# Optimization experiments

Hardware: AMD Instinct MI355X
Metric: run time of the kernel (lower is better)

## Reference

```python
import jax, jax.numpy as jnp
import numpy as np
from jax import lax

N = 64          # padded / uniform graph size
B = 512         # number of graph pairs
E = 512         # edges per graph
GCN_SIZES = [64, 32, 16]
CONV_OUT = [8, 16, 32]
D_IN = 16


def gcn_conv(x, src, dst, W, b):
    # PyG GCNConv: add self-loops, symmetric norm D^-1/2 (A+I) D^-1/2, then XW + b
    n = x.shape[0]
    h = x @ W
    deg = jnp.zeros((n,), x.dtype).at[dst].add(1.0) + 1.0  # +1 self-loop
    dinv = lax.rsqrt(deg)
    msg = h[src] * (dinv[src] * dinv[dst])[:, None]
    agg = jnp.zeros_like(h).at[dst].add(msg) + h * (dinv * dinv)[:, None]
    return agg + b


def gcn_pass(x, ei, Ws, bs):
    src, dst = ei[0], ei[1]
    feats = []
    h = x
    for i in range(len(Ws)):
        h = gcn_conv(h, src, dst, Ws[i], bs[i])
        feats.append(h)               # pre-ReLU features are used for similarity
        if i < len(Ws) - 1:
            h = jax.nn.relu(h)        # dropout p used in eval -> identity
    return feats


def conv_same(x, w, b):
    y = lax.conv_general_dilated(x, w, (1, 1), 'SAME',
                                 dimension_numbers=('NCHW', 'OIHW', 'NCHW'))
    return y + b[None, :, None, None]


def maxpool2(x):
    return lax.reduce_window(x, -jnp.inf, lax.max, (1, 1, 2, 2), (1, 1, 2, 2), 'VALID')


def setup_inputs() -> dict:
    key = jax.random.key(0)
    ks = jax.random.split(key, 32)
    f32 = jnp.float32
    x_q = jax.random.normal(ks[0], (B * N, D_IN), f32)
    x_c = jax.random.normal(ks[1], (B * N, D_IN), f32)
    off = (jnp.arange(B, dtype=jnp.int32) * N)[:, None]
    eq_s = (jax.random.randint(ks[2], (B, E), 0, N, jnp.int32) + off).reshape(-1)
    eq_d = (jax.random.randint(ks[3], (B, E), 0, N, jnp.int32) + off).reshape(-1)
    ec_s = (jax.random.randint(ks[4], (B, E), 0, N, jnp.int32) + off).reshape(-1)
    ec_d = (jax.random.randint(ks[5], (B, E), 0, N, jnp.int32) + off).reshape(-1)
    edge_q = jnp.stack([eq_s, eq_d])
    edge_c = jnp.stack([ec_s, ec_d])

    def lin(k, fi, fo):
        return jax.random.normal(k, (fi, fo), f32) / np.sqrt(fi)

    inp = dict(x_q=x_q, x_c=x_c, edge_q=edge_q, edge_c=edge_c)
    dims = [D_IN] + GCN_SIZES
    for i in range(3):
        inp[f'gcn_w{i+1}'] = lin(ks[6 + i], dims[i], dims[i + 1])
        inp[f'gcn_b{i+1}'] = jnp.zeros((dims[i + 1],), f32)
    cin = [1] + CONV_OUT[:-1]
    for i in range(3):
        fan = cin[i] * 25
        inp[f'conv_w{i+1}'] = jax.random.normal(ks[10 + i], (3, CONV_OUT[i], cin[i], 5, 5), f32) / np.sqrt(fan)
        inp[f'conv_b{i+1}'] = jnp.zeros((3, CONV_OUT[i]), f32)
    inp['lin_w1'] = lin(ks[14], 6144, 256)
    inp['lin_b1'] = jnp.zeros((256,), f32)
    inp['lin_w2'] = lin(ks[15], 256, 16)
    inp['lin_b2'] = jnp.zeros((16,), f32)
    inp['score_w'] = lin(ks[16], 16, 1)
    inp['score_b'] = jnp.zeros((1,), f32)
    return inp


def _forward(x_q, x_c, gcn_w1, gcn_b1, gcn_w2, gcn_b2, gcn_w3, gcn_b3,
             conv_w1, conv_b1, conv_w2, conv_b2, conv_w3, conv_b3,
             lin_w1, lin_b1, lin_w2, lin_b2, score_w, score_b,
             edge_q, edge_c):
    Ws = (gcn_w1, gcn_w2, gcn_w3)
    bs = (gcn_b1, gcn_b2, gcn_b3)
    qf = gcn_pass(x_q, edge_q, Ws, bs)   # list of [B*N, d_i]
    cf = gcn_pass(x_c, edge_c, Ws, bs)
    sims = [jnp.einsum('bnd,bmd->bnm', q.reshape(B, N, -1), c.reshape(B, N, -1))
            for q, c in zip(qf, cf)]
    cw = (conv_w1, conv_w2, conv_w3)
    cb = (conv_b1, conv_b2, conv_b3)
    outs = []
    for m in range(3):                    # separate conv weights per similarity matrix
        z = sims[m][:, None]              # [B, 1, N, N]
        for l in range(3):
            z = maxpool2(jax.nn.relu(conv_same(z, cw[l][m], cb[l][m])))
        outs.append(z)                    # [B, 32, 8, 8]
    feat = jnp.concatenate(outs, axis=1).reshape(B, 6144)
    h = jax.nn.relu(feat @ lin_w1 + lin_b1)
    h = jax.nn.relu(h @ lin_w2 + lin_b2)
    return (h @ score_w + score_b).reshape(-1)  # is_sig=False -> logits [B]


def reference(x_q, x_c, edge_q, edge_c, gcn_w1, gcn_b1, gcn_w2, gcn_b2, gcn_w3, gcn_b3,
              conv_w1, conv_b1, conv_w2, conv_b2, conv_w3, conv_b3,
              lin_w1, lin_b1, lin_w2, lin_b2, score_w, score_b):
    return _forward(x_q, x_c, gcn_w1, gcn_b1, gcn_w2, gcn_b2, gcn_w3, gcn_b3,
                    conv_w1, conv_b1, conv_w2, conv_b2, conv_w3, conv_b3,
                    lin_w1, lin_b1, lin_w2, lin_b2, score_w, score_b,
                    edge_q, edge_c)
```

## Files before the change

### kernel.cpp

```cpp
#include <hip/hip_runtime.h>
#include <hip/hip_bf16.h>

constexpr int B = 512, N = 64, E = 512, NE = B * E;

typedef __attribute__((ext_vector_type(8))) short bf8v;
typedef __attribute__((ext_vector_type(4))) float f32x4;
typedef unsigned short u16;

__device__ __forceinline__ u16 f2bf(float f) {
  unsigned u = __builtin_bit_cast(unsigned, f);
  u += 0x7FFFu + ((u >> 16) & 1u);
  return (u16)(u >> 16);
}

__device__ __forceinline__ int cmin(int a, int b) { return a < b ? a : b; }

template <int DIN, int DOUT, int NR, int NC, bool STORE_NEXT>
__device__ __forceinline__ void gcn_layer(
    float* __restrict__ At, float* __restrict__ Xt, float* __restrict__ Hs,
    const float* __restrict__ W, const float* __restrict__ bias,
    u16* __restrict__ fout, int g, int t) {
  constexpr int XS = 68;
  constexpr int CT = DOUT / NC;
  static_assert((64 / NR) * CT == 512, "thread mapping");
  const int ct = t % CT, nt = t / CT;
  const int n0 = NR * nt, c0 = NC * ct;
  {
    float acc[NR][NC] = {};
#pragma unroll 4
    for (int k = 0; k < DIN; ++k) {
      float xa[NR];
      if constexpr (NR == 4) {
        float4 xv = *(const float4*)&Xt[k * XS + n0];
        xa[0] = xv.x; xa[1] = xv.y; xa[2] = xv.z; xa[3] = xv.w;
      } else {
        float2 xv = *(const float2*)&Xt[k * XS + n0];
        xa[0] = xv.x; xa[1] = xv.y;
      }
      float wa[NC];
      if constexpr (NC == 2) {
        float2 wv = *(const float2*)&W[k * DOUT + c0];
        wa[0] = wv.x; wa[1] = wv.y;
      } else {
        wa[0] = W[k * DOUT + c0];
      }
#pragma unroll
      for (int i = 0; i < NR; ++i)
#pragma unroll
        for (int j = 0; j < NC; ++j) acc[i][j] += xa[i] * wa[j];
    }
#pragma unroll
    for (int i = 0; i < NR; ++i) {
      if constexpr (NC == 2)
        *(float2*)&Hs[(n0 + i) * XS + c0] = make_float2(acc[i][0], acc[i][1]);
      else
        Hs[(n0 + i) * XS + c0] = acc[i][0];
    }
  }
  __syncthreads();
  {
    float acc[NR][NC] = {};
#pragma unroll 4
    for (int s = 0; s < N; ++s) {
      float aa[NR];
      if constexpr (NR == 4) {
        float4 av = *(const float4*)&At[s * XS + n0];
        aa[0] = av.x; aa[1] = av.y; aa[2] = av.z; aa[3] = av.w;
      } else {
        float2 av = *(const float2*)&At[s * XS + n0];
        aa[0] = av.x; aa[1] = av.y;
      }
      float ha[NC];
      if constexpr (NC == 2) {
        float2 hv = *(const float2*)&Hs[s * XS + c0];
        ha[0] = hv.x; ha[1] = hv.y;
      } else {
        ha[0] = Hs[s * XS + c0];
      }
#pragma unroll
      for (int i = 0; i < NR; ++i)
#pragma unroll
        for (int j = 0; j < NC; ++j) acc[i][j] += aa[i] * ha[j];
    }
    float bv[NC];
#pragma unroll
    for (int j = 0; j < NC; ++j) bv[j] = bias[c0 + j];
#pragma unroll
    for (int i = 0; i < NR; ++i) {
      float st[NC];
#pragma unroll
      for (int j = 0; j < NC; ++j) st[j] = acc[i][j] + bv[j];
      if constexpr (NC == 2) {
        unsigned pack = (unsigned)f2bf(st[0]) | ((unsigned)f2bf(st[1]) << 16);
        *(unsigned*)&fout[(size_t)g * N * DOUT + (size_t)(n0 + i) * DOUT + c0] = pack;
      } else {
        fout[(size_t)g * N * DOUT + (size_t)(n0 + i) * DOUT + c0] = f2bf(st[0]);
      }
      if (STORE_NEXT) {
#pragma unroll
        for (int j = 0; j < NC; ++j)
          Xt[(c0 + j) * XS + n0 + i] = fmaxf(st[j], 0.f);
      }
    }
  }
  __syncthreads();
}

__global__ __launch_bounds__(512) void gcn_fused(
    const float* __restrict__ xq, const float* __restrict__ xc,
    const float* __restrict__ W1, const float* __restrict__ b1,
    const float* __restrict__ W2, const float* __restrict__ b2,
    const float* __restrict__ W3, const float* __restrict__ b3,
    const int* __restrict__ eq, const int* __restrict__ ec,
    u16* __restrict__ f1q, u16* __restrict__ f1c,
    u16* __restrict__ f2q, u16* __restrict__ f2c,
    u16* __restrict__ f3q, u16* __restrict__ f3c) {
  constexpr int XS = 68;
  __shared__ __align__(16) float At[N * XS];
  __shared__ __align__(16) float Xt[N * XS];
  __shared__ __align__(16) float Hs[N * XS];
  __shared__ float dl[N];
  __shared__ int cnt[N];
  const int g = blockIdx.x, t = threadIdx.x;
  const float* x = blockIdx.y ? xc : xq;
  const int* edges = blockIdx.y ? ec : eq;
  u16* o1 = blockIdx.y ? f1c : f1q;
  u16* o2 = blockIdx.y ? f2c : f2q;
  u16* o3 = blockIdx.y ? f3c : f3q;
  for (int i = t; i < N * 16; i += 512) {
    int n = i / 16, k = i % 16;
    Xt[k * XS + n] = x[(size_t)g * N * 16 + i];
  }
  for (int i = t; i < N * XS; i += 512) At[i] = 0.f;
  if (t < N) cnt[t] = 1;
  __syncthreads();
  const int* srcp = edges + (size_t)g * E;
  const int* dstp = edges + NE + (size_t)g * E;
  for (int j = t; j < E; j += 512) atomicAdd(&cnt[dstp[j] & 63], 1);
  __syncthreads();
  if (t < N) dl[t] = rsqrtf((float)cnt[t]);
  __syncthreads();
  for (int j = t; j < E; j += 512) {
    int s = srcp[j] & 63, d = dstp[j] & 63;
    atomicAdd(&At[s * XS + d], dl[s] * dl[d]);
  }
  if (t < N) atomicAdd(&At[t * XS + t], dl[t] * dl[t]);
  __syncthreads();
  gcn_layer<16, 64, 4, 2, true>(At, Xt, Hs, W1, b1, o1, g, t);
  gcn_layer<64, 32, 4, 1, true>(At, Xt, Hs, W2, b2, o2, g, t);
  gcn_layer<32, 16, 2, 1, false>(At, Xt, Hs, W3, b3, o3, g, t);
}

__global__ __launch_bounds__(256, 4) void simconv1(
    const u16* __restrict__ f1q, const u16* __restrict__ f1c,
    const u16* __restrict__ f2q, const u16* __restrict__ f2c,
    const u16* __restrict__ f3q, const u16* __restrict__ f3c,
    const float* __restrict__ w, const float* __restrict__ bias,
    u16* __restrict__ out) {
  constexpr int PS = 68, QS = 72;
  __shared__ __align__(16) u16 Qs[64 * QS];
  __shared__ __align__(16) u16 Cs[64 * QS];
  __shared__ __align__(16) float simp[68 * 68];
  __shared__ float wls[25 * 8];
  __shared__ float bls[8];
  const int b = blockIdx.x, m = blockIdx.y, t = threadIdx.x;
  for (int i = t; i < 68 * 68; i += 256) simp[i] = 0.f;
  if (t < 200) {
    int oc = t / 25, tap = t % 25;
    wls[tap * 8 + oc] = w[m * 200 + t];
  }
  if (t < 8) bls[t] = bias[m * 8 + t];
  const u16* fq = (m == 0) ? f1q : (m == 1) ? f2q : f3q;
  const u16* fc = (m == 0) ? f1c : (m == 1) ? f2c : f3c;
  const int D = 64 >> m;
  const int SEG = D >> 3;
  for (int i = t; i < 64 * SEG; i += 256) {
    int n = i / SEG, s = i - n * SEG;
    *(uint4*)&Qs[n * QS + s * 8] = *(const uint4*)&fq[(size_t)b * 64 * D + n * D + s * 8];
    *(uint4*)&Cs[n * QS + s * 8] = *(const uint4*)&fc[(size_t)b * 64 * D + n * D + s * 8];
  }
  if (m == 2 && t < 128) {
    int n = t >> 1, s = t & 1;
    uint4 z = {0u, 0u, 0u, 0u};
    *(uint4*)&Qs[n * QS + 16 + s * 8] = z;
    *(uint4*)&Cs[n * QS + 16 + s * 8] = z;
  }
  __syncthreads();
  const int w4 = t >> 6, lane = t & 63;
  const int r16 = lane & 15, kg = lane >> 4;
  const int Kpad = (m == 0) ? 64 : 32;
#pragma unroll 1
  for (int ct = 0; ct < 4; ++ct) {
    f32x4 acc = {0.f, 0.f, 0.f, 0.f};
    for (int ks = 0; ks < Kpad; ks += 32) {
      bf8v a = *(const bf8v*)&Qs[(w4 * 16 + r16) * QS + ks + kg * 8];
      bf8v bb = *(const bf8v*)&Cs[(ct * 16 + r16) * QS + ks + kg * 8];
      acc = __builtin_amdgcn_mfma_f32_16x16x32_bf16(a, bb, acc, 0, 0, 0);
    }
#pragma unroll
    for (int j = 0; j < 4; ++j)
      simp[(w4 * 16 + kg * 4 + j + 2) * PS + ct * 16 + r16 + 2] = acc[j];
  }
  __syncthreads();
  const int gy = t >> 4, gx = t & 15;
  float pr[8][8];
#pragma unroll
  for (int yy = 0; yy < 8; ++yy) {
    float4 a = *(const float4*)&simp[(4 * gy + yy) * PS + 4 * gx];
    float4 bb = *(const float4*)&simp[(4 * gy + yy) * PS + 4 * gx + 4];
    pr[yy][0] = a.x; pr[yy][1] = a.y; pr[yy][2] = a.z; pr[yy][3] = a.w;
    pr[yy][4] = bb.x; pr[yy][5] = bb.y; pr[yy][6] = bb.z; pr[yy][7] = bb.w;
  }
  u16* op = out + (size_t)(b * 3 + m) * 8192;
#pragma unroll 1
  for (int p2 = 0; p2 < 4; ++p2) {
    float acc[2][16];
#pragma unroll
    for (int p = 0; p < 16; ++p) { acc[0][p] = 0.f; acc[1][p] = 0.f; }
#pragma unroll
    for (int ky = 0; ky < 5; ++ky)
#pragma unroll
      for (int kx = 0; kx < 5; ++kx) {
        float2 wv = *(const float2*)&wls[(ky * 5 + kx) * 8 + p2 * 2];
#pragma unroll
        for (int dy = 0; dy < 4; ++dy)
#pragma unroll
          for (int dx = 0; dx < 4; ++dx) {
            float rv = pr[ky + dy][kx + dx];
            acc[0][dy * 4 + dx] += rv * wv.x;
            acc[1][dy * 4 + dx] += rv * wv.y;
          }
      }
    float b0 = bls[p2 * 2], b1 = bls[p2 * 2 + 1];
#pragma unroll
    for (int ay = 0; ay < 2; ++ay)
#pragma unroll
      for (int ax = 0; ax < 2; ++ax) {
        float v0 = fmaxf(fmaxf(acc[0][(2 * ay) * 4 + 2 * ax], acc[0][(2 * ay) * 4 + 2 * ax + 1]),
                         fmaxf(acc[0][(2 * ay + 1) * 4 + 2 * ax], acc[0][(2 * ay + 1) * 4 + 2 * ax + 1]));
        float v1 = fmaxf(fmaxf(acc[1][(2 * ay) * 4 + 2 * ax], acc[1][(2 * ay) * 4 + 2 * ax + 1]),
                         fmaxf(acc[1][(2 * ay + 1) * 4 + 2 * ax], acc[1][(2 * ay + 1) * 4 + 2 * ax + 1]));
        v0 = fmaxf(v0 + b0, 0.f);
        v1 = fmaxf(v1 + b1, 0.f);
        unsigned pack = (unsigned)f2bf(v0) | ((unsigned)f2bf(v1) << 16);
        *(unsigned*)&op[(size_t)(((2 * gy + ay) * 32) + (2 * gx + ax)) * 8 + p2 * 2] = pack;
      }
  }
}

__global__ __launch_bounds__(256) void prep_kernel(
    const float* __restrict__ lw1, const float* __restrict__ cw2,
    const float* __restrict__ cw3, u16* __restrict__ wT,
    u16* __restrict__ w2p, u16* __restrict__ w3p) {
  const int t = threadIdx.x;
  if (blockIdx.x < 384) {
    __shared__ float tile[64][65];
    const int k0 = (blockIdx.x % 96) * 64, c0 = (blockIdx.x / 96) * 64;
    for (int i = t; i < 4096; i += 256) {
      int r = i >> 6, c = i & 63;
      tile[r][c] = lw1[(size_t)(k0 + r) * 256 + c0 + c];
    }
    __syncthreads();
    for (int i = t; i < 4096; i += 256) {
      int c = i >> 6, k = i & 63;
      wT[(size_t)(c0 + c) * 6144 + k0 + k] = f2bf(tile[k][c]);
    }
    return;
  }
  int i = (blockIdx.x - 384) * 256 + t;
  if (i < 3 * 7 * 16 * 40) {
    int m = i / 4480, r = i % 4480;
    int k = r % 40, rest = r / 40, oc = rest & 15, st = rest >> 4;
    u16 v = 0;
    if (k < 32) {
      int sl = k >> 3, ci = k & 7, tap = st * 4 + sl;
      if (tap < 25) v = f2bf(cw2[((size_t)(m * 16 + oc) * 8 + ci) * 25 + tap]);
    }
    w2p[i] = v;
  }
  if (i < 3 * 26 * 16 * 40) {
    int m = i / 16640, r = i % 16640;
    int k = r % 40, rest = r / 40, oc16 = rest & 15, sthalf = rest >> 4;
    int half = sthalf & 1, st = sthalf >> 1;
    u16 v = 0;
    if (k < 32) {
      int sl = k >> 4, ci = k & 15, tap = st * 2 + sl;
      int oc = half * 16 + oc16;
      if (tap < 25) v = f2bf(cw3[((size_t)(m * 32 + oc) * 16 + ci) * 25 + tap]);
    }
    w3p[i] = v;
  }
}

__global__ __launch_bounds__(256) void conv23_mfma(
    const u16* __restrict__ in, const u16* __restrict__ w2p,
    const float* __restrict__ cb2, const u16* __restrict__ w3p,
    const float* __restrict__ cb3, u16* __restrict__ feat) {
  constexpr int PW2 = 36, PW3 = 20, BS = 40;
  __shared__ __align__(16) u16 uni[16640];
  __shared__ __align__(16) u16 p2s[PW3 * PW3 * 16];
  __shared__ float bls2[16];
  __shared__ float bls3[32];
  const int b = blockIdx.x, m = blockIdx.y, t = threadIdx.x;
  u16* ins2 = uni;
  u16* w2ls = uni + 10368;
  const size_t ibase = (size_t)(b * 3 + m) * 8192;
  for (int i = t; i < PW2 * PW2; i += 256) {
    int y = i / PW2, x = i % PW2;
    uint4 v = {0u, 0u, 0u, 0u};
    if (y >= 2 && y < 34 && x >= 2 && x < 34)
      v = *(const uint4*)&in[ibase + (size_t)((y - 2) * 32 + (x - 2)) * 8];
    *(uint4*)&ins2[i * 8] = v;
  }
  {
    const u16* wsrc = w2p + m * 4480;
    for (int i = t; i < 560; i += 256) *(uint4*)&w2ls[i * 8] = *(const uint4*)&wsrc[i * 8];
  }
  {
    uint4 z = {0u, 0u, 0u, 0u};
    for (int i = t; i < 800; i += 256) *(uint4*)&p2s[i * 8] = z;
  }
  if (t < 16) bls2[t] = cb2[m * 16 + t];
  if (t >= 32 && t < 64) bls3[t - 32] = cb3[m * 32 + (t - 32)];
  __syncthreads();
  const int wv = t >> 6, lane = t & 63;
  const int oc = lane & 15, g = lane >> 4;
  {
    const int xt = wv & 1, ypb = wv >> 1;
    const int x = xt * 16 + oc;
    __builtin_amdgcn_s_setprio(1);
#pragma unroll 1
    for (int grp = 0; grp < 2; ++grp) {
      f32x4 acc[4][2];
#pragma unroll
      for (int i = 0; i < 4; ++i) {
        acc[i][0] = (f32x4){0.f, 0.f, 0.f, 0.f};
        acc[i][1] = (f32x4){0.f, 0.f, 0.f, 0.f};
      }
#pragma unroll
      for (int st = 0; st < 7; ++st) {
        bf8v bvv = *(const bf8v*)&w2ls[(st * 16 + oc) * BS + g * 8];
        const int c0 = cmin(st * 4 + 0, 24), c1 = cmin(st * 4 + 1, 24);
        const int c2 = cmin(st * 4 + 2, 24), c3 = cmin(st * 4 + 3, 24);
        const int k0 = (c0 / 5) * PW2 + c0 % 5, k1 = (c1 / 5) * PW2 + c1 % 5;
        const int k2 = (c2 / 5) * PW2 + c2 % 5, k3 = (c3 / 5) * PW2 + c3 % 5;
        const int koff = (g == 0) ? k0 : (g == 1) ? k1 : (g == 2) ? k2 : k3;
#pragma unroll
        for (int i = 0; i < 4; ++i) {
          const int y0 = 2 * ypb + 4 * (grp * 4 + i);
          const int abase = (y0 * PW2 + x + koff) * 8;
          bf8v a0 = *(const bf8v*)&ins2[abase];
          acc[i][0] = __builtin_amdgcn_mfma_f32_16x16x32_bf16(a0, bvv, acc[i][0], 0, 0, 0);
          bf8v a1 = *(const bf8v*)&ins2[abase + PW2 * 8];
          acc[i][1] = __builtin_amdgcn_mfma_f32_16x16x32_bf16(a1, bvv, acc[i][1], 0, 0, 0);
        }
      }
      const float bb = bls2[oc];
#pragma unroll
      for (int i = 0; i < 4; ++i) {
        const int yp = ypb + 2 * (grp * 4 + i);
        const float v0 = fmaxf(fmaxf(fmaxf(acc[i][0][0], acc[i][0][1]),
                                     fmaxf(acc[i][1][0], acc[i][1][1])) + bb, 0.f);
        const float v1 = fmaxf(fmaxf(fmaxf(acc[i][0][2], acc[i][0][3]),
                                     fmaxf(acc[i][1][2], acc[i][1][3])) + bb, 0.f);
        const int px = xt * 8 + 2 * g;
        p2s[((yp + 2) * PW3 + (px + 2)) * 16 + oc] = f2bf(v0);
        p2s[((yp + 2) * PW3 + (px + 3)) * 16 + oc] = f2bf(v1);
      }
    }
    __builtin_amdgcn_s_setprio(0);
  }
  __syncthreads();
  {
    const u16* wsrc = w3p + m * 16640;
    for (int i = t; i < 2080; i += 256) *(uint4*)&uni[i * 8] = *(const uint4*)&wsrc[i * 8];
  }
  __syncthreads();
  {
    const int sl = g >> 1, ch = (g & 1) * 8;
    const int half = wv & 1, ypb = wv >> 1;
    u16* fb = feat + (size_t)b * 6144 + m * 2048;
    f32x4 acc[4][2];
#pragma unroll
    for (int i = 0; i < 4; ++i) {
      acc[i][0] = (f32x4){0.f, 0.f, 0.f, 0.f};
      acc[i][1] = (f32x4){0.f, 0.f, 0.f, 0.f};
    }
    __builtin_amdgcn_s_setprio(1);
#pragma unroll
    for (int st = 0; st < 13; ++st) {
      bf8v bvv = *(const bf8v*)&uni[(size_t)((st * 2 + half) * 16 + oc) * BS + g * 8];
      const int c0 = cmin(st * 2 + 0, 24), c1 = cmin(st * 2 + 1, 24);
      const int k0 = (c0 / 5) * PW3 + c0 % 5, k1 = (c1 / 5) * PW3 + c1 % 5;
      const int koff = sl ? k1 : k0;
#pragma unroll
      for (int i = 0; i < 4; ++i) {
        const int y0 = 2 * ypb + 4 * i;
        const int abase = (y0 * PW3 + oc + koff) * 16 + ch;
        bf8v a0 = *(const bf8v*)&p2s[abase];
        acc[i][0] = __builtin_amdgcn_mfma_f32_16x16x32_bf16(a0, bvv, acc[i][0], 0, 0, 0);
        bf8v a1 = *(const bf8v*)&p2s[abase + PW3 * 16];
        acc[i][1] = __builtin_amdgcn_mfma_f32_16x16x32_bf16(a1, bvv, acc[i][1], 0, 0, 0);
      }
    }
    __builtin_amdgcn_s_setprio(0);
    const int ocg = half * 16 + oc;
    const float bb = bls3[ocg];
#pragma unroll
    for (int i = 0; i < 4; ++i) {
      const int yp = ypb + 2 * i;
      const float v0 = fmaxf(fmaxf(fmaxf(acc[i][0][0], acc[i][0][1]),
                                   fmaxf(acc[i][1][0], acc[i][1][1])) + bb, 0.f);
      const float v1 = fmaxf(fmaxf(fmaxf(acc[i][0][2], acc[i][0][3]),
                                   fmaxf(acc[i][1][2], acc[i][1][3])) + bb, 0.f);
      unsigned pack = (unsigned)f2bf(v0) | ((unsigned)f2bf(v1) << 16);
      *(unsigned*)&fb[ocg * 64 + yp * 8 + 2 * g] = pack;
    }
  }
}

__global__ __launch_bounds__(256) void lin1_mfma(const u16* __restrict__ feat,
                                                 const u16* __restrict__ wT,
                                                 float* __restrict__ h1p) {
  constexpr int AS = 72;
  __shared__ __align__(16) u16 As[64 * AS];
  __shared__ __align__(16) u16 Bs[64 * AS];
  const int r0 = blockIdx.x * 64, c0 = blockIdx.y * 64, kb = blockIdx.z * 384;
  const int t = threadIdx.x;
  const int w = t >> 6, lane = t & 63;
  const int row16 = lane & 15, kg = lane >> 4;
  f32x4 acc[4] = {{0.f, 0.f, 0.f, 0.f}, {0.f, 0.f, 0.f, 0.f},
                  {0.f, 0.f, 0.f, 0.f}, {0.f, 0.f, 0.f, 0.f}};
  const int lr = t >> 2, lk = (t & 3) * 16;
#pragma unroll 1
  for (int st = 0; st < 6; ++st) {
    __syncthreads();
    const int ks = kb + st * 64;
    {
      const u16* srcA = feat + (size_t)(r0 + lr) * 6144 + ks + lk;
      uint4 a0 = *(const uint4*)srcA;
      uint4 a1 = *(const uint4*)(srcA + 8);
      *(uint4*)&As[lr * AS + lk] = a0;
      *(uint4*)&As[lr * AS + lk + 8] = a1;
      const u16* srcB = wT + (size_t)(c0 + lr) * 6144 + ks + lk;
      uint4 b0 = *(const uint4*)srcB;
      uint4 b1 = *(const uint4*)(srcB + 8);
      *(uint4*)&Bs[lr * AS + lk] = b0;
      *(uint4*)&Bs[lr * AS + lk + 8] = b1;
    }
    __syncthreads();
#pragma unroll
    for (int kk = 0; kk < 2; ++kk) {
      bf8v a = *(const bf8v*)&As[(w * 16 + row16) * AS + kk * 32 + kg * 8];
#pragma unroll
      for (int ct = 0; ct < 4; ++ct) {
        bf8v bb = *(const bf8v*)&Bs[(ct * 16 + row16) * AS + kk * 32 + kg * 8];
        acc[ct] = __builtin_amdgcn_mfma_f32_16x16x32_bf16(a, bb, acc[ct], 0, 0, 0);
      }
    }
  }
  float* out = h1p + (size_t)blockIdx.z * 131072;
#pragma unroll
  for (int ct = 0; ct < 4; ++ct)
#pragma unroll
    for (int j = 0; j < 4; ++j)
      out[(size_t)(r0 + w * 16 + kg * 4 + j) * 256 + c0 + ct * 16 + row16] = acc[ct][j];
}

__global__ __launch_bounds__(256) void head_kernel(
    const float* __restrict__ h1p, const float* __restrict__ b1,
    const float* __restrict__ w2, const float* __restrict__ b2,
    const float* __restrict__ sw, const float* __restrict__ sb,
    float* __restrict__ out) {
  constexpr int HS = 260;
  __shared__ __align__(16) float h1s[16 * HS];
  __shared__ __align__(16) float w2s[256 * 16];
  const int r0 = blockIdx.x * 16, t = threadIdx.x;
  for (int i = t; i < 4096; i += 256) {
    int r = i >> 8, k = i & 255;
    float s = b1[k];
#pragma unroll
    for (int p = 0; p < 16; ++p) s += h1p[(size_t)p * 131072 + (size_t)(r0 + r) * 256 + k];
    h1s[r * HS + k] = s;
    w2s[i] = w2[i];
  }
  __syncthreads();
  const int j = t & 15, r = t >> 4;
  float acc = b2[j];
#pragma unroll 4
  for (int k4 = 0; k4 < 64; ++k4) {
    float4 hv = *(const float4*)&h1s[r * HS + 4 * k4];
    float h0 = fmaxf(hv.x, 0.f), h1v = fmaxf(hv.y, 0.f);
    float h2v = fmaxf(hv.z, 0.f), h3 = fmaxf(hv.w, 0.f);
    acc += h0 * w2s[(4 * k4 + 0) * 16 + j];
    acc += h1v * w2s[(4 * k4 + 1) * 16 + j];
    acc += h2v * w2s[(4 * k4 + 2) * 16 + j];
    acc += h3 * w2s[(4 * k4 + 3) * 16 + j];
  }
  float v = fmaxf(acc, 0.f) * sw[j];
#pragma unroll
  for (int off = 8; off; off >>= 1) v += __shfl_xor(v, off, 16);
  if (j == 0) out[r0 + r] = v + sb[0];
}

extern "C" void kernel_launch(void* const* d_in, const int* in_sizes, int n_in,
                              void* d_out, int out_size, void* d_ws, size_t ws_size,
                              hipStream_t stream) {
  const float* x_q = (const float*)d_in[0];
  const float* x_c = (const float*)d_in[1];
  const int* edge_q = (const int*)d_in[2];
  const int* edge_c = (const int*)d_in[3];
  const float* gw1 = (const float*)d_in[4];
  const float* gb1 = (const float*)d_in[5];
  const float* gw2 = (const float*)d_in[6];
  const float* gb2 = (const float*)d_in[7];
  const float* gw3 = (const float*)d_in[8];
  const float* gb3 = (const float*)d_in[9];
  const float* cw1 = (const float*)d_in[10];
  const float* cb1 = (const float*)d_in[11];
  const float* cw2 = (const float*)d_in[12];
  const float* cb2 = (const float*)d_in[13];
  const float* cw3 = (const float*)d_in[14];
  const float* cb3 = (const float*)d_in[15];
  const float* lw1 = (const float*)d_in[16];
  const float* lb1 = (const float*)d_in[17];
  const float* lw2 = (const float*)d_in[18];
  const float* lb2 = (const float*)d_in[19];
  const float* swt = (const float*)d_in[20];
  const float* sbs = (const float*)d_in[21];
  float* ws = (float*)d_ws;

  const size_t o_f1q = 65536;
  const size_t o_f2q = o_f1q + 2097152;
  const size_t o_f3q = o_f2q + 1048576;
  const size_t o_f1c = o_f3q + 524288;
  const size_t o_f2c = o_f1c + 2097152;
  const size_t o_f3c = o_f2c + 1048576;
  const size_t o_sims = o_f3c + 524288;
  const size_t o_pm1 = o_sims + 6291456;
  const size_t o_pm2 = o_pm1 + 6291456;
  const size_t o_wT = o_pm2 + 3145728;
  const size_t o_w2p = o_wT + 786432;
  const size_t o_w3p = o_w2p + 8192;
  const size_t o_feat = o_sims;
  const size_t o_h1p = o_f1q;

  u16* f1q = (u16*)(ws + o_f1q); u16* f2q = (u16*)(ws + o_f2q); u16* f3q = (u16*)(ws + o_f3q);
  u16* f1c = (u16*)(ws + o_f1c); u16* f2c = (u16*)(ws + o_f2c); u16* f3c = (u16*)(ws + o_f3c);
  u16* pm1 = (u16*)(ws + o_pm1);
  u16* wT = (u16*)(ws + o_wT);
  u16* w2p = (u16*)(ws + o_w2p);
  u16* w3p = (u16*)(ws + o_w3p);
  u16* feat = (u16*)(ws + o_feat);
  float* h1p = ws + o_h1p;

  prep_kernel<<<580, 256, 0, stream>>>(lw1, cw2, cw3, wT, w2p, w3p);

  gcn_fused<<<dim3(B, 2), 512, 0, stream>>>(x_q, x_c, gw1, gb1, gw2, gb2, gw3, gb3,
                                            edge_q, edge_c, f1q, f1c, f2q, f2c, f3q, f3c);

  simconv1<<<dim3(B, 3), 256, 0, stream>>>(f1q, f1c, f2q, f2c, f3q, f3c, cw1, cb1, pm1);

  conv23_mfma<<<dim3(B, 3), 256, 0, stream>>>(pm1, w2p, cb2, w3p, cb3, feat);

  lin1_mfma<<<dim3(8, 4, 16), 256, 0, stream>>>(feat, wT, h1p);
  head_kernel<<<32, 256, 0, stream>>>(h1p, lb1, lw2, lb2, swt, sbs, (float*)d_out);
}
```

Measured before the change: 131.0 us.

## Rewrite fused GCN layers with bf16 MFMA in a 256-thread block

Replaces the scalar fp32 FMA loops for both the XW and the normalized-adjacency matmuls in the GCN kernel with 16x16x32 bf16 MFMA instructions. Adjacency, features and intermediate H are stored in shared memory as bf16 with padded rows, weights are converted and transposed into shared memory per layer, and the block shrinks from 512 to 256 threads. The aim is to cut the ALU cost of the per-graph GCN stage. In exchange, intermediate activations and the adjacency are rounded to bf16, which loses precision, and the per-layer weight staging adds an extra barrier.

```diff
diff --git a/kernel.cpp b/kernel.cpp
--- a/kernel.cpp
+++ b/kernel.cpp
@@ -15,98 +15,59 @@
 
 __device__ __forceinline__ int cmin(int a, int b) { return a < b ? a : b; }
 
-template <int DIN, int DOUT, int NR, int NC, bool STORE_NEXT>
-__device__ __forceinline__ void gcn_layer(
-    float* __restrict__ At, float* __restrict__ Xt, float* __restrict__ Hs,
-    const float* __restrict__ W, const float* __restrict__ bias,
-    u16* __restrict__ fout, int g, int t) {
-  constexpr int XS = 68;
-  constexpr int CT = DOUT / NC;
-  static_assert((64 / NR) * CT == 512, "thread mapping");
-  const int ct = t % CT, nt = t / CT;
-  const int n0 = NR * nt, c0 = NC * ct;
-  {
-    float acc[NR][NC] = {};
-#pragma unroll 4
-    for (int k = 0; k < DIN; ++k) {
-      float xa[NR];
-      if constexpr (NR == 4) {
-        float4 xv = *(const float4*)&Xt[k * XS + n0];
-        xa[0] = xv.x; xa[1] = xv.y; xa[2] = xv.z; xa[3] = xv.w;
-      } else {
-        float2 xv = *(const float2*)&Xt[k * XS + n0];
-        xa[0] = xv.x; xa[1] = xv.y;
-      }
-      float wa[NC];
-      if constexpr (NC == 2) {
-        float2 wv = *(const float2*)&W[k * DOUT + c0];
-        wa[0] = wv.x; wa[1] = wv.y;
-      } else {
-        wa[0] = W[k * DOUT + c0];
-      }
-#pragma unroll
-      for (int i = 0; i < NR; ++i)
-#pragma unroll
-        for (int j = 0; j < NC; ++j) acc[i][j] += xa[i] * wa[j];
-    }
-#pragma unroll
-    for (int i = 0; i < NR; ++i) {
-      if constexpr (NC == 2)
-        *(float2*)&Hs[(n0 + i) * XS + c0] = make_float2(acc[i][0], acc[i][1]);
-      else
-        Hs[(n0 + i) * XS + c0] = acc[i][0];
-    }
-  }
-  __syncthreads();
-  {
-    float acc[NR][NC] = {};
-#pragma unroll 4
-    for (int s = 0; s < N; ++s) {
-      float aa[NR];
-      if constexpr (NR == 4) {
-        float4 av = *(const float4*)&At[s * XS + n0];
-        aa[0] = av.x; aa[1] = av.y; aa[2] = av.z; aa[3] = av.w;
-      } else {
-        float2 av = *(const float2*)&At[s * XS + n0];
-        aa[0] = av.x; aa[1] = av.y;
-      }
-      float ha[NC];
-      if constexpr (NC == 2) {
-        float2 hv = *(const float2*)&Hs[s * XS + c0];
-        ha[0] = hv.x; ha[1] = hv.y;
-      } else {
-        ha[0] = Hs[s * XS + c0];
-      }
-#pragma unroll
-      for (int i = 0; i < NR; ++i)
-#pragma unroll
-        for (int j = 0; j < NC; ++j) acc[i][j] += aa[i] * ha[j];
-    }
-    float bv[NC];
-#pragma unroll
-    for (int j = 0; j < NC; ++j) bv[j] = bias[c0 + j];
-#pragma unroll
-    for (int i = 0; i < NR; ++i) {
-      float st[NC];
-#pragma unroll
-      for (int j = 0; j < NC; ++j) st[j] = acc[i][j] + bv[j];
-      if constexpr (NC == 2) {
-        unsigned pack = (unsigned)f2bf(st[0]) | ((unsigned)f2bf(st[1]) << 16);
-        *(unsigned*)&fout[(size_t)g * N * DOUT + (size_t)(n0 + i) * DOUT + c0] = pack;
-      } else {
-        fout[(size_t)g * N * DOUT + (size_t)(n0 + i) * DOUT + c0] = f2bf(st[0]);
-      }
-      if (STORE_NEXT) {
-#pragma unroll
-        for (int j = 0; j < NC; ++j)
-          Xt[(c0 + j) * XS + n0 + i] = fmaxf(st[j], 0.f);
-      }
-    }
-  }
-  __syncthreads();
-}
-
-__global__ __launch_bounds__(512) void gcn_fused(
+template <int DIN, int KP, int DOUT, bool STORE_NEXT>
+__device__ __forceinline__ void gcn_layer_mfma(
+    const u16* __restrict__ Ab, u16* __restrict__ Xb, u16* __restrict__ Hb,
+    u16* __restrict__ Wb, const float* __restrict__ W,
+    const float* __restrict__ bias, u16* __restrict__ fout, int g, int t) {
+  for (int i = t; i < DOUT * KP; i += 256) {
+    int c = i / KP, k = i % KP;
+    u16 v = 0;
+    if (k < DIN) v = f2bf(W[k * DOUT + c]);
+    Wb[c * 72 + k] = v;
+  }
+  __syncthreads();
+  const int w4 = t >> 6, lane = t & 63;
+  const int r16 = lane & 15, kg = lane >> 4;
+  constexpr int CT = DOUT / 16;
+#pragma unroll
+  for (int ct = 0; ct < CT; ++ct) {
+    f32x4 acc = {0.f, 0.f, 0.f, 0.f};
+#pragma unroll
+    for (int ks = 0; ks < KP; ks += 32) {
+      bf8v a = *(const bf8v*)&Xb[(w4 * 16 + r16) * 72 + ks + kg * 8];
+      bf8v bb = *(const bf8v*)&Wb[(ct * 16 + r16) * 72 + ks + kg * 8];
+      acc = __builtin_amdgcn_mfma_f32_16x16x32_bf16(a, bb, acc, 0, 0, 0);
+    }
+    ushort4 pk;
+    pk.x = f2bf(acc[0]); pk.y = f2bf(acc[1]);
+    pk.z = f2bf(acc[2]); pk.w = f2bf(acc[3]);
+    *(ushort4*)&Hb[(ct * 16 + r16) * 72 + w4 * 16 + kg * 4] = pk;
+  }
+  __syncthreads();
+#pragma unroll
+  for (int ct = 0; ct < CT; ++ct) {
+    f32x4 acc = {0.f, 0.f, 0.f, 0.f};
+#pragma unroll
+    for (int ks = 0; ks < 64; ks += 32) {
+      bf8v a = *(const bf8v*)&Ab[(w4 * 16 + r16) * 72 + ks + kg * 8];
+      bf8v bb = *(const bf8v*)&Hb[(ct * 16 + r16) * 72 + ks + kg * 8];
+      acc = __builtin_amdgcn_mfma_f32_16x16x32_bf16(a, bb, acc, 0, 0, 0);
+    }
+    const int c = ct * 16 + r16;
+    const float bv = bias[c];
+#pragma unroll
+    for (int j = 0; j < 4; ++j) {
+      float st = acc[j] + bv;
+      const int d = w4 * 16 + kg * 4 + j;
+      fout[(size_t)g * N * DOUT + (size_t)d * DOUT + c] = f2bf(st);
+      if (STORE_NEXT) Xb[d * 72 + c] = f2bf(fmaxf(st, 0.f));
+    }
+  }
+  __syncthreads();
+}
+
+__global__ __launch_bounds__(256) void gcn_fused(
     const float* __restrict__ xq, const float* __restrict__ xc,
     const float* __restrict__ W1, const float* __restrict__ b1,
     const float* __restrict__ W2, const float* __restrict__ b2,
@@ -115,40 +76,48 @@
     u16* __restrict__ f1q, u16* __restrict__ f1c,
     u16* __restrict__ f2q, u16* __restrict__ f2c,
     u16* __restrict__ f3q, u16* __restrict__ f3c) {
-  constexpr int XS = 68;
-  __shared__ __align__(16) float At[N * XS];
-  __shared__ __align__(16) float Xt[N * XS];
-  __shared__ __align__(16) float Hs[N * XS];
+  __shared__ __align__(16) float Af[64 * 68];
+  __shared__ __align__(16) u16 Ab[64 * 72];
+  __shared__ __align__(16) u16 Xb[64 * 72];
+  __shared__ __align__(16) u16 Hb[64 * 72];
   __shared__ float dl[N];
   __shared__ int cnt[N];
+  u16* Wb = (u16*)Af;
   const int g = blockIdx.x, t = threadIdx.x;
   const float* x = blockIdx.y ? xc : xq;
   const int* edges = blockIdx.y ? ec : eq;
   u16* o1 = blockIdx.y ? f1c : f1q;
   u16* o2 = blockIdx.y ? f2c : f2q;
   u16* o3 = blockIdx.y ? f3c : f3q;
-  for (int i = t; i < N * 16; i += 512) {
-    int n = i / 16, k = i % 16;
-    Xt[k * XS + n] = x[(size_t)g * N * 16 + i];
-  }
-  for (int i = t; i < N * XS; i += 512) At[i] = 0.f;
+  for (int i = t; i < 64 * 32; i += 256) {
+    int n = i >> 5, k = i & 31;
+    u16 v = 0;
+    if (k < 16) v = f2bf(x[(size_t)g * 1024 + n * 16 + k]);
+    Xb[n * 72 + k] = v;
+  }
+  for (int i = t; i < 64 * 68; i += 256) Af[i] = 0.f;
   if (t < N) cnt[t] = 1;
   __syncthreads();
   const int* srcp = edges + (size_t)g * E;
   const int* dstp = edges + NE + (size_t)g * E;
-  for (int j = t; j < E; j += 512) atomicAdd(&cnt[dstp[j] & 63], 1);
+  for (int j = t; j < E; j += 256) atomicAdd(&cnt[dstp[j] & 63], 1);
   __syncthreads();
   if (t < N) dl[t] = rsqrtf((float)cnt[t]);
   __syncthreads();
-  for (int j = t; j < E; j += 512) {
+  for (int j = t; j < E; j += 256) {
     int s = srcp[j] & 63, d = dstp[j] & 63;
-    atomicAdd(&At[s * XS + d], dl[s] * dl[d]);
-  }
-  if (t < N) atomicAdd(&At[t * XS + t], dl[t] * dl[t]);
-  __syncthreads();
-  gcn_layer<16, 64, 4, 2, true>(At, Xt, Hs, W1, b1, o1, g, t);
-  gcn_layer<64, 32, 4, 1, true>(At, Xt, Hs, W2, b2, o2, g, t);
-  gcn_layer<32, 16, 2, 1, false>(At, Xt, Hs, W3, b3, o3, g, t);
+    atomicAdd(&Af[d * 68 + s], dl[s] * dl[d]);
+  }
+  if (t < N) atomicAdd(&Af[t * 68 + t], dl[t] * dl[t]);
+  __syncthreads();
+  for (int i = t; i < 4096; i += 256) {
+    int d = i >> 6, s = i & 63;
+    Ab[d * 72 + s] = f2bf(Af[d * 68 + s]);
+  }
+  __syncthreads();
+  gcn_layer_mfma<16, 32, 64, true>(Ab, Xb, Hb, Wb, W1, b1, o1, g, t);
+  gcn_layer_mfma<64, 64, 32, true>(Ab, Xb, Hb, Wb, W2, b2, o2, g, t);
+  gcn_layer_mfma<32, 32, 16, false>(Ab, Xb, Hb, Wb, W3, b3, o3, g, t);
 }
 
 __global__ __launch_bounds__(256, 4) void simconv1(
@@ -556,7 +525,7 @@
 
   prep_kernel<<<580, 256, 0, stream>>>(lw1, cw2, cw3, wT, w2p, w3p);
 
-  gcn_fused<<<dim3(B, 2), 512, 0, stream>>>(x_q, x_c, gw1, gb1, gw2, gb2, gw3, gb3,
+  gcn_fused<<<dim3(B, 2), 256, 0, stream>>>(x_q, x_c, gw1, gb1, gw2, gb2, gw3, gb3,
                                             edge_q, edge_c, f1q, f1c, f2q, f2c, f3q, f3c);
 
   simconv1<<<dim3(B, 3), 256, 0, stream>>>(f1q, f1c, f2q, f2c, f3q, f3c, cw1, cb1, pm1);
```

Measured after the change: 121.1 us (median of 2 runs). 1.08x faster.
